# Kernel tuning notes

Measured on AMD Instinct MI355X. Metric: run time of the kernel, lower is better.

Reference implementation:

```python
import jax, jax.numpy as jnp
import numpy as np
import math

B, T, IN_DIM, HID = 32, 1024, 512, 512
TAU_MEM = 20.0
THRESHOLD = 1.0
ALPHA = math.exp(-1.0 / TAU_MEM)


def setup_inputs() -> dict:
    key = jax.random.key(0)
    kx, kw, kb = jax.random.split(key, 3)
    bound = 1.0 / math.sqrt(IN_DIM)
    x = jax.random.normal(kx, (B, T, IN_DIM), dtype=jnp.float32)
    W = jax.random.uniform(kw, (HID, IN_DIM), minval=-bound, maxval=bound, dtype=jnp.float32)
    b = jax.random.uniform(kb, (HID,), minval=-bound, maxval=bound, dtype=jnp.float32)
    threshold_adapt = jnp.ones((HID,), dtype=jnp.float32) * THRESHOLD
    return {"x": x, "W": W, "b": b, "threshold_adapt": threshold_adapt}


def reference(x, W, b, threshold_adapt):
    # Precompute the batched GEMM for all timesteps: z[b,t,h]
    z = jnp.einsum('bti,hi->bth', x, W) + b
    thr = threshold_adapt[None, :]  # [1,H]

    def step(mem, z_t):
        # leaky integrate
        mem = ALPHA * mem + z_t              # [B,H]
        spike = (mem >= thr).astype(mem.dtype)
        mem = mem * (1.0 - spike)            # hard reset
        return mem, spike

    mem0 = jnp.zeros((x.shape[0], W.shape[0]), dtype=x.dtype)
    # scan over time axis: z transposed to [T,B,H]
    mem_final, spikes = jax.lax.scan(step, mem0, jnp.swapaxes(z, 0, 1))
    spikes = jnp.swapaxes(spikes, 0, 1)      # [B,T,H]
    return spikes, mem_final
```

## Files before the change

### kernel.cpp

```cpp
#include <hip/hip_runtime.h>
#include <cstdint>
#include <cstddef>

#define BATCH  32
#define TSTEPS 1024
#define INDIM  512
#define HIDDIM 512
#define MTOT   (BATCH * TSTEPS)

#define MB 128
#define NB 128
#define KC 32
#define KTILES (INDIM / KC)
#define NBLK   (HIDDIM / NB)

constexpr float ALPHA = 0.951229424500714f;

__global__ __launch_bounds__(256)
void snn_gemm(const float* __restrict__ x, const float* __restrict__ W,
              float* __restrict__ z)
{
    __shared__ float Asm[KC][MB];
    __shared__ float Bsm[KC][NB];

    const int tid = threadIdx.x;
    const int mb  = blockIdx.x / NBLK;
    const int nb  = blockIdx.x % NBLK;
    const int m0  = mb * MB;
    const int n0  = nb * NB;

    const int sr = tid >> 1;
    const int sc = (tid & 1) * 4;

    const float4* Ag = reinterpret_cast<const float4*>(x + (size_t)(m0 + sr) * INDIM) + sc;
    const float4* Bg = reinterpret_cast<const float4*>(W + (size_t)(n0 + sr) * INDIM) + sc;

    const int cm = (tid >> 4) * 8;
    const int cn = (tid & 15) * 8;

    float acc[8][8];
#pragma unroll
    for (int i = 0; i < 8; ++i)
#pragma unroll
        for (int j = 0; j < 8; ++j) acc[i][j] = 0.0f;

    float4 sa[4], sb[4];
#pragma unroll
    for (int j = 0; j < 4; ++j) { sa[j] = Ag[j]; sb[j] = Bg[j]; }

    for (int kt = 0; kt < KTILES; ++kt) {
        __syncthreads();
#pragma unroll
        for (int j = 0; j < 4; ++j) {
            const int kq = (sc + j) * 4;
            Asm[kq + 0][sr] = sa[j].x;
            Asm[kq + 1][sr] = sa[j].y;
            Asm[kq + 2][sr] = sa[j].z;
            Asm[kq + 3][sr] = sa[j].w;
            Bsm[kq + 0][sr] = sb[j].x;
            Bsm[kq + 1][sr] = sb[j].y;
            Bsm[kq + 2][sr] = sb[j].z;
            Bsm[kq + 3][sr] = sb[j].w;
        }
        __syncthreads();

        if (kt + 1 < KTILES) {
            Ag += KC / 4;
            Bg += KC / 4;
#pragma unroll
            for (int j = 0; j < 4; ++j) { sa[j] = Ag[j]; sb[j] = Bg[j]; }
        }

#pragma unroll 8
        for (int kc = 0; kc < KC; ++kc) {
            float4 a0 = *reinterpret_cast<const float4*>(&Asm[kc][cm]);
            float4 a1 = *reinterpret_cast<const float4*>(&Asm[kc][cm + 4]);
            float4 b0 = *reinterpret_cast<const float4*>(&Bsm[kc][cn]);
            float4 b1 = *reinterpret_cast<const float4*>(&Bsm[kc][cn + 4]);
            const float av[8] = {a0.x, a0.y, a0.z, a0.w, a1.x, a1.y, a1.z, a1.w};
            const float bv[8] = {b0.x, b0.y, b0.z, b0.w, b1.x, b1.y, b1.z, b1.w};
#pragma unroll
            for (int i = 0; i < 8; ++i)
#pragma unroll
                for (int j = 0; j < 8; ++j)
                    acc[i][j] = fmaf(av[i], bv[j], acc[i][j]);
        }
    }

#pragma unroll
    for (int i = 0; i < 8; ++i) {
        float* zr = z + (size_t)(m0 + cm + i) * HIDDIM + n0 + cn;
        float4 v0 = {acc[i][0], acc[i][1], acc[i][2], acc[i][3]};
        float4 v1 = {acc[i][4], acc[i][5], acc[i][6], acc[i][7]};
        *reinterpret_cast<float4*>(zr)     = v0;
        *reinterpret_cast<float4*>(zr + 4) = v1;
    }
}

template <bool INPLACE>
__global__ __launch_bounds__(64)
void snn_scan(const float* zsrc, float* out,
              const float* __restrict__ bias, const float* __restrict__ thr)
{
    const int h = (blockIdx.x & 7) * 64 + threadIdx.x;
    const int b = blockIdx.x >> 3;

    const float bb = bias[h];
    const float tt = thr[h];
    float mem = 0.0f;

    const size_t base = ((size_t)b * TSTEPS) * HIDDIM + h;
    const float* zp = zsrc + base;
    float* sp = out + base;

    for (int t = 0; t < TSTEPS; t += 8) {
        float zl[8];
#pragma unroll
        for (int j = 0; j < 8; ++j)
            zl[j] = zp[(size_t)(t + j) * HIDDIM];
#pragma unroll
        for (int j = 0; j < 8; ++j) {
            float zv = zl[j] + bb;
            mem = fmaf(ALPHA, mem, zv);
            bool s = (mem >= tt);
            sp[(size_t)(t + j) * HIDDIM] = s ? 1.0f : 0.0f;
            mem = s ? 0.0f : mem;
        }
    }
    out[(size_t)MTOT * HIDDIM + (size_t)b * HIDDIM + h] = mem;
}

extern "C" void kernel_launch(void* const* d_in, const int* in_sizes, int n_in,
                              void* d_out, int out_size, void* d_ws, size_t ws_size,
                              hipStream_t stream)
{
    const float* x    = (const float*)d_in[0];
    const float* W    = (const float*)d_in[1];
    const float* bias = (const float*)d_in[2];
    const float* thr  = (const float*)d_in[3];
    float* out = (float*)d_out;

    (void)in_sizes; (void)n_in; (void)out_size;

    const size_t z_bytes = (size_t)MTOT * HIDDIM * sizeof(float);
    float* zbuf;
    bool use_ws = (ws_size >= z_bytes);
    zbuf = use_ws ? (float*)d_ws : out;

    dim3 ggrid((MTOT / MB) * NBLK);
    hipLaunchKernelGGL(snn_gemm, ggrid, dim3(256), 0, stream, x, W, zbuf);

    dim3 sgrid(BATCH * (HIDDIM / 64));
    if (use_ws)
        hipLaunchKernelGGL((snn_scan<false>), sgrid, dim3(64), 0, stream, zbuf, out, bias, thr);
    else
        hipLaunchKernelGGL((snn_scan<true>),  sgrid, dim3(64), 0, stream, zbuf, out, bias, thr);
}
```

Baseline: 389.9 us.

## Enlarge GEMM tile with swizzled LDS and double-buffer scan via async global-to-LDS loads

The GEMM moves to 256x128 tiles with 16x8 per-thread accumulators and XOR-swizzled shared-memory columns, cutting bank conflicts and raising arithmetic intensity per LDS read. The scan kernel becomes 256-thread blocks that prefetch 64-timestep chunks of z into LDS with global_load_lds double buffering, hiding the latency of the serial recurrence. The risks are register pressure from 128 accumulators under a 2-blocks launch bound, and far fewer scan blocks (64), which limits parallelism across the GPU.

```diff
diff --git a/kernel.cpp b/kernel.cpp
--- a/kernel.cpp
+++ b/kernel.cpp
@@ -8,79 +8,105 @@
 #define HIDDIM 512
 #define MTOT   (BATCH * TSTEPS)
 
-#define MB 128
-#define NB 128
-#define KC 32
-#define KTILES (INDIM / KC)
-#define NBLK   (HIDDIM / NB)
+#define GMB 256
+#define GNB 128
+#define GKC 32
+#define GKT (INDIM / GKC)
+#define GNBLK (HIDDIM / GNB)
+
+#define SB_H 256
+#define SB_T 64
+#define SB_NC (TSTEPS / SB_T)
 
 constexpr float ALPHA = 0.951229424500714f;
 
-__global__ __launch_bounds__(256)
+__device__ __forceinline__ int swzA(int g) { return g ^ (g >> 3); }
+__device__ __forceinline__ int swzB(int g) { return g ^ (g >> 3); }
+
+__global__ __launch_bounds__(256, 2)
 void snn_gemm(const float* __restrict__ x, const float* __restrict__ W,
               float* __restrict__ z)
 {
-    __shared__ float Asm[KC][MB];
-    __shared__ float Bsm[KC][NB];
+    __shared__ float Asm[GKC][GMB];
+    __shared__ float Bsm[GKC][GNB];
 
     const int tid = threadIdx.x;
-    const int mb  = blockIdx.x / NBLK;
-    const int nb  = blockIdx.x % NBLK;
-    const int m0  = mb * MB;
-    const int n0  = nb * NB;
-
-    const int sr = tid >> 1;
-    const int sc = (tid & 1) * 4;
-
-    const float4* Ag = reinterpret_cast<const float4*>(x + (size_t)(m0 + sr) * INDIM) + sc;
-    const float4* Bg = reinterpret_cast<const float4*>(W + (size_t)(n0 + sr) * INDIM) + sc;
-
-    const int cm = (tid >> 4) * 8;
+    const int mb  = blockIdx.x / GNBLK;
+    const int nb  = blockIdx.x % GNBLK;
+    const int m0  = mb * GMB;
+    const int n0  = nb * GNB;
+
+    const float4* Ag = reinterpret_cast<const float4*>(x + (size_t)(m0 + tid) * INDIM);
+    const int   acol = (swzA(tid >> 2) << 2) | (tid & 3);
+    const int   brow = tid & 127;
+    const int   bkq  = (tid >> 7) * 4;
+    const float4* Bg = reinterpret_cast<const float4*>(W + (size_t)(n0 + brow) * INDIM) + bkq;
+    const int   bcol = (swzB(brow >> 2) << 2) | (brow & 3);
+
+    const int cm = (tid >> 4) * 16;
     const int cn = (tid & 15) * 8;
-
-    float acc[8][8];
-#pragma unroll
-    for (int i = 0; i < 8; ++i)
+    int pa[4], pb[2];
+#pragma unroll
+    for (int i = 0; i < 4; ++i) pa[i] = swzA((cm >> 2) + i);
+#pragma unroll
+    for (int j = 0; j < 2; ++j) pb[j] = swzB((cn >> 2) + j);
+
+    float acc[16][8];
+#pragma unroll
+    for (int i = 0; i < 16; ++i)
 #pragma unroll
         for (int j = 0; j < 8; ++j) acc[i][j] = 0.0f;
 
-    float4 sa[4], sb[4];
-#pragma unroll
-    for (int j = 0; j < 4; ++j) { sa[j] = Ag[j]; sb[j] = Bg[j]; }
-
-    for (int kt = 0; kt < KTILES; ++kt) {
+    float4 sa[8], sb[4];
+#pragma unroll
+    for (int q = 0; q < 8; ++q) sa[q] = Ag[q];
+#pragma unroll
+    for (int q = 0; q < 4; ++q) sb[q] = Bg[q];
+
+    for (int kt = 0; kt < GKT; ++kt) {
         __syncthreads();
 #pragma unroll
-        for (int j = 0; j < 4; ++j) {
-            const int kq = (sc + j) * 4;
-            Asm[kq + 0][sr] = sa[j].x;
-            Asm[kq + 1][sr] = sa[j].y;
-            Asm[kq + 2][sr] = sa[j].z;
-            Asm[kq + 3][sr] = sa[j].w;
-            Bsm[kq + 0][sr] = sb[j].x;
-            Bsm[kq + 1][sr] = sb[j].y;
-            Bsm[kq + 2][sr] = sb[j].z;
-            Bsm[kq + 3][sr] = sb[j].w;
+        for (int q = 0; q < 8; ++q) {
+            const int k4 = q * 4;
+            Asm[k4 + 0][acol] = sa[q].x;
+            Asm[k4 + 1][acol] = sa[q].y;
+            Asm[k4 + 2][acol] = sa[q].z;
+            Asm[k4 + 3][acol] = sa[q].w;
+        }
+#pragma unroll
+        for (int q = 0; q < 4; ++q) {
+            const int k4 = (bkq + q) * 4;
+            Bsm[k4 + 0][bcol] = sb[q].x;
+            Bsm[k4 + 1][bcol] = sb[q].y;
+            Bsm[k4 + 2][bcol] = sb[q].z;
+            Bsm[k4 + 3][bcol] = sb[q].w;
         }
         __syncthreads();
 
-        if (kt + 1 < KTILES) {
-            Ag += KC / 4;
-            Bg += KC / 4;
-#pragma unroll
-            for (int j = 0; j < 4; ++j) { sa[j] = Ag[j]; sb[j] = Bg[j]; }
-        }
-
-#pragma unroll 8
-        for (int kc = 0; kc < KC; ++kc) {
-            float4 a0 = *reinterpret_cast<const float4*>(&Asm[kc][cm]);
-            float4 a1 = *reinterpret_cast<const float4*>(&Asm[kc][cm + 4]);
-            float4 b0 = *reinterpret_cast<const float4*>(&Bsm[kc][cn]);
-            float4 b1 = *reinterpret_cast<const float4*>(&Bsm[kc][cn + 4]);
-            const float av[8] = {a0.x, a0.y, a0.z, a0.w, a1.x, a1.y, a1.z, a1.w};
-            const float bv[8] = {b0.x, b0.y, b0.z, b0.w, b1.x, b1.y, b1.z, b1.w};
-#pragma unroll
-            for (int i = 0; i < 8; ++i)
+        if (kt + 1 < GKT) {
+            Ag += GKC / 4;
+            Bg += GKC / 4;
+#pragma unroll
+            for (int q = 0; q < 8; ++q) sa[q] = Ag[q];
+#pragma unroll
+            for (int q = 0; q < 4; ++q) sb[q] = Bg[q];
+        }
+
+#pragma unroll 4
+        for (int kc = 0; kc < GKC; ++kc) {
+            const float4* Ar = reinterpret_cast<const float4*>(&Asm[kc][0]);
+            const float4* Br = reinterpret_cast<const float4*>(&Bsm[kc][0]);
+            float4 a0 = Ar[pa[0]];
+            float4 a1 = Ar[pa[1]];
+            float4 a2 = Ar[pa[2]];
+            float4 a3 = Ar[pa[3]];
+            float4 b0 = Br[pb[0]];
+            float4 b1 = Br[pb[1]];
+            const float av[16] = {a0.x, a0.y, a0.z, a0.w, a1.x, a1.y, a1.z, a1.w,
+                                  a2.x, a2.y, a2.z, a2.w, a3.x, a3.y, a3.z, a3.w};
+            const float bv[8]  = {b0.x, b0.y, b0.z, b0.w, b1.x, b1.y, b1.z, b1.w};
+#pragma unroll
+            for (int i = 0; i < 16; ++i)
 #pragma unroll
                 for (int j = 0; j < 8; ++j)
                     acc[i][j] = fmaf(av[i], bv[j], acc[i][j]);
@@ -88,7 +114,7 @@
     }
 
 #pragma unroll
-    for (int i = 0; i < 8; ++i) {
+    for (int i = 0; i < 16; ++i) {
         float* zr = z + (size_t)(m0 + cm + i) * HIDDIM + n0 + cn;
         float4 v0 = {acc[i][0], acc[i][1], acc[i][2], acc[i][3]};
         float4 v1 = {acc[i][4], acc[i][5], acc[i][6], acc[i][7]};
@@ -97,37 +123,67 @@
     }
 }
 
-template <bool INPLACE>
-__global__ __launch_bounds__(64)
-void snn_scan(const float* zsrc, float* out,
+__global__ __launch_bounds__(256)
+void snn_scan(const float* __restrict__ zsrc, float* __restrict__ out,
               const float* __restrict__ bias, const float* __restrict__ thr)
 {
-    const int h = (blockIdx.x & 7) * 64 + threadIdx.x;
-    const int b = blockIdx.x >> 3;
-
-    const float bb = bias[h];
-    const float tt = thr[h];
+    __shared__ float zl[2][SB_T][SB_H];
+
+    const int tid  = threadIdx.x;
+    const int lane = tid & 63;
+    const int wave = tid >> 6;
+    const int b    = blockIdx.x >> 1;
+    const int h0   = (blockIdx.x & 1) * SB_H;
+
+    const float bb = bias[h0 + tid];
+    const float tt = thr[h0 + tid];
     float mem = 0.0f;
 
-    const size_t base = ((size_t)b * TSTEPS) * HIDDIM + h;
-    const float* zp = zsrc + base;
-    float* sp = out + base;
-
-    for (int t = 0; t < TSTEPS; t += 8) {
-        float zl[8];
-#pragma unroll
-        for (int j = 0; j < 8; ++j)
-            zl[j] = zp[(size_t)(t + j) * HIDDIM];
-#pragma unroll
-        for (int j = 0; j < 8; ++j) {
-            float zv = zl[j] + bb;
+    const float* zbase = zsrc + (size_t)b * TSTEPS * HIDDIM + h0;
+    float*       obase = out  + (size_t)b * TSTEPS * HIDDIM + h0;
+
+    auto issue = [&](int c, int buf) {
+        const float* gr = zbase + ((size_t)c * SB_T + wave * 16) * HIDDIM + lane * 4;
+        const float* lr = &zl[buf][wave * 16][0];
+#pragma unroll
+        for (int r = 0; r < 16; ++r) {
+            __builtin_amdgcn_global_load_lds(
+                (const __attribute__((address_space(1))) void*)gr,
+                (__attribute__((address_space(3))) void*)lr, 16, 0, 0);
+            gr += HIDDIM;
+            lr += SB_H;
+        }
+    };
+
+    issue(0, 0);
+
+    for (int c = 0; c < SB_NC; ++c) {
+        const int buf = c & 1;
+        if (c + 1 < SB_NC) {
+            issue(c + 1, buf ^ 1);
+            asm volatile("s_waitcnt vmcnt(16)" ::: "memory");
+        } else {
+            asm volatile("s_waitcnt vmcnt(0)" ::: "memory");
+        }
+        __builtin_amdgcn_sched_barrier(0);
+        __builtin_amdgcn_s_barrier();
+
+        float* orow = obase + (size_t)c * SB_T * HIDDIM + tid;
+#pragma unroll 8
+        for (int r = 0; r < SB_T; ++r) {
+            float zv = zl[buf][r][tid] + bb;
             mem = fmaf(ALPHA, mem, zv);
             bool s = (mem >= tt);
-            sp[(size_t)(t + j) * HIDDIM] = s ? 1.0f : 0.0f;
+            orow[(size_t)r * HIDDIM] = s ? 1.0f : 0.0f;
             mem = s ? 0.0f : mem;
         }
+
+        asm volatile("s_waitcnt lgkmcnt(0)" ::: "memory");
+        __builtin_amdgcn_sched_barrier(0);
+        __builtin_amdgcn_s_barrier();
     }
-    out[(size_t)MTOT * HIDDIM + (size_t)b * HIDDIM + h] = mem;
+
+    out[(size_t)MTOT * HIDDIM + (size_t)b * HIDDIM + h0 + tid] = mem;
 }
 
 extern "C" void kernel_launch(void* const* d_in, const int* in_sizes, int n_in,
@@ -143,16 +199,11 @@
     (void)in_sizes; (void)n_in; (void)out_size;
 
     const size_t z_bytes = (size_t)MTOT * HIDDIM * sizeof(float);
-    float* zbuf;
-    bool use_ws = (ws_size >= z_bytes);
-    zbuf = use_ws ? (float*)d_ws : out;
-
-    dim3 ggrid((MTOT / MB) * NBLK);
+    float* zbuf = (ws_size >= z_bytes) ? (float*)d_ws : out;
+
+    dim3 ggrid((MTOT / GMB) * GNBLK);
     hipLaunchKernelGGL(snn_gemm, ggrid, dim3(256), 0, stream, x, W, zbuf);
 
-    dim3 sgrid(BATCH * (HIDDIM / 64));
-    if (use_ws)
-        hipLaunchKernelGGL((snn_scan<false>), sgrid, dim3(64), 0, stream, zbuf, out, bias, thr);
-    else
-        hipLaunchKernelGGL((snn_scan<true>),  sgrid, dim3(64), 0, stream, zbuf, out, bias, thr);
+    dim3 sgrid(BATCH * (HIDDIM / SB_H));
+    hipLaunchKernelGGL(snn_scan, sgrid, dim3(256), 0, stream, zbuf, out, bias, thr);
 }
```

Result: faster. 374.2 us (-4.0%).

## Double-buffer GEMM LDS with swizzle and pipeline scan via async LDS loads

Applied to the files above, without the earlier changes.

The GEMM now double-buffers its shared-memory tiles, which removes one barrier per k-tile, and XOR-swizzles the LDS layout to cut bank conflicts on the transposed stores. The scan kernel now streams 64-timestep chunks of z into LDS with global_load_lds, double-buffered and governed by explicit vmcnt waits. Spikes are staged in LDS and written out as coalesced float4 rows. The scan previously ran 256 threads-per-block-equivalent strided scalar loads with little latency hiding. In exchange, the in-place fallback that wrote z into out loses its aliasing safety because restrict is now asserted, and the hand-coded waitcnt values are fragile.

```diff
diff --git a/kernel.cpp b/kernel.cpp
--- a/kernel.cpp
+++ b/kernel.cpp
@@ -11,17 +11,23 @@
 #define MB 128
 #define NB 128
 #define KC 32
-#define KTILES (INDIM / KC)
-#define NBLK   (HIDDIM / NB)
+#define KT (INDIM / KC)
+#define NBLK (HIDDIM / NB)
+
+#define SH 64
+#define ST 64
+#define SNC (TSTEPS / ST)
 
 constexpr float ALPHA = 0.951229424500714f;
+
+__device__ __forceinline__ int swzg(int g) { return g ^ (g >> 3); }
 
 __global__ __launch_bounds__(256)
 void snn_gemm(const float* __restrict__ x, const float* __restrict__ W,
               float* __restrict__ z)
 {
-    __shared__ float Asm[KC][MB];
-    __shared__ float Bsm[KC][NB];
+    __shared__ float Asm[2][KC][MB];
+    __shared__ float Bsm[2][KC][NB];
 
     const int tid = threadIdx.x;
     const int mb  = blockIdx.x / NBLK;
@@ -31,12 +37,15 @@
 
     const int sr = tid >> 1;
     const int sc = (tid & 1) * 4;
+    const int swr = (swzg(sr >> 2) << 2) | (sr & 3);
 
     const float4* Ag = reinterpret_cast<const float4*>(x + (size_t)(m0 + sr) * INDIM) + sc;
     const float4* Bg = reinterpret_cast<const float4*>(W + (size_t)(n0 + sr) * INDIM) + sc;
 
     const int cm = (tid >> 4) * 8;
     const int cn = (tid & 15) * 8;
+    const int am0 = swzg(cm >> 2), am1 = swzg((cm >> 2) + 1);
+    const int bn0 = swzg(cn >> 2), bn1 = swzg((cn >> 2) + 1);
 
     float acc[8][8];
 #pragma unroll
@@ -45,38 +54,48 @@
         for (int j = 0; j < 8; ++j) acc[i][j] = 0.0f;
 
     float4 sa[4], sb[4];
-#pragma unroll
-    for (int j = 0; j < 4; ++j) { sa[j] = Ag[j]; sb[j] = Bg[j]; }
-
-    for (int kt = 0; kt < KTILES; ++kt) {
-        __syncthreads();
-#pragma unroll
-        for (int j = 0; j < 4; ++j) {
-            const int kq = (sc + j) * 4;
-            Asm[kq + 0][sr] = sa[j].x;
-            Asm[kq + 1][sr] = sa[j].y;
-            Asm[kq + 2][sr] = sa[j].z;
-            Asm[kq + 3][sr] = sa[j].w;
-            Bsm[kq + 0][sr] = sb[j].x;
-            Bsm[kq + 1][sr] = sb[j].y;
-            Bsm[kq + 2][sr] = sb[j].z;
-            Bsm[kq + 3][sr] = sb[j].w;
-        }
-        __syncthreads();
-
-        if (kt + 1 < KTILES) {
-            Ag += KC / 4;
-            Bg += KC / 4;
-#pragma unroll
-            for (int j = 0; j < 4; ++j) { sa[j] = Ag[j]; sb[j] = Bg[j]; }
-        }
-
+
+    auto gload = [&]() {
+#pragma unroll
+        for (int q = 0; q < 4; ++q) { sa[q] = Ag[q]; sb[q] = Bg[q]; }
+        Ag += KC / 4;
+        Bg += KC / 4;
+    };
+    auto lwrite = [&](int p) {
+#pragma unroll
+        for (int q = 0; q < 4; ++q) {
+            const int kq = (sc + q) * 4;
+            Asm[p][kq + 0][swr] = sa[q].x;
+            Asm[p][kq + 1][swr] = sa[q].y;
+            Asm[p][kq + 2][swr] = sa[q].z;
+            Asm[p][kq + 3][swr] = sa[q].w;
+            Bsm[p][kq + 0][swr] = sb[q].x;
+            Bsm[p][kq + 1][swr] = sb[q].y;
+            Bsm[p][kq + 2][swr] = sb[q].z;
+            Bsm[p][kq + 3][swr] = sb[q].w;
+        }
+    };
+
+    gload();
+    lwrite(0);
+    __syncthreads();
+    gload();
+
+    for (int kt = 0; kt < KT; ++kt) {
+        const int p = kt & 1;
+        if (kt + 1 < KT) lwrite(p ^ 1);
+        if (kt + 2 < KT) gload();
+
+        const float (*Ap)[MB] = Asm[p];
+        const float (*Bp)[NB] = Bsm[p];
 #pragma unroll 8
         for (int kc = 0; kc < KC; ++kc) {
-            float4 a0 = *reinterpret_cast<const float4*>(&Asm[kc][cm]);
-            float4 a1 = *reinterpret_cast<const float4*>(&Asm[kc][cm + 4]);
-            float4 b0 = *reinterpret_cast<const float4*>(&Bsm[kc][cn]);
-            float4 b1 = *reinterpret_cast<const float4*>(&Bsm[kc][cn + 4]);
+            const float4* Ar = reinterpret_cast<const float4*>(&Ap[kc][0]);
+            const float4* Br = reinterpret_cast<const float4*>(&Bp[kc][0]);
+            float4 a0 = Ar[am0];
+            float4 a1 = Ar[am1];
+            float4 b0 = Br[bn0];
+            float4 b1 = Br[bn1];
             const float av[8] = {a0.x, a0.y, a0.z, a0.w, a1.x, a1.y, a1.z, a1.w};
             const float bv[8] = {b0.x, b0.y, b0.z, b0.w, b1.x, b1.y, b1.z, b1.w};
 #pragma unroll
@@ -85,6 +104,7 @@
                 for (int j = 0; j < 8; ++j)
                     acc[i][j] = fmaf(av[i], bv[j], acc[i][j]);
         }
+        if (kt + 1 < KT) __syncthreads();
     }
 
 #pragma unroll
@@ -97,37 +117,71 @@
     }
 }
 
-template <bool INPLACE>
 __global__ __launch_bounds__(64)
-void snn_scan(const float* zsrc, float* out,
+void snn_scan(const float* __restrict__ zsrc, float* __restrict__ out,
               const float* __restrict__ bias, const float* __restrict__ thr)
 {
-    const int h = (blockIdx.x & 7) * 64 + threadIdx.x;
-    const int b = blockIdx.x >> 3;
-
-    const float bb = bias[h];
-    const float tt = thr[h];
+    __shared__ float zl[2][ST][SH];
+    __shared__ float stile[ST][SH];
+
+    const int lane = threadIdx.x;
+    const int b    = blockIdx.x >> 3;
+    const int h0   = (blockIdx.x & 7) * SH;
+
+    const float* zbase = zsrc + (size_t)b * TSTEPS * HIDDIM + h0;
+    float*       obase = out  + (size_t)b * TSTEPS * HIDDIM + h0;
+
+    const float bb = bias[h0 + lane];
+    const float tt = thr[h0 + lane];
     float mem = 0.0f;
 
-    const size_t base = ((size_t)b * TSTEPS) * HIDDIM + h;
-    const float* zp = zsrc + base;
-    float* sp = out + base;
-
-    for (int t = 0; t < TSTEPS; t += 8) {
-        float zl[8];
-#pragma unroll
-        for (int j = 0; j < 8; ++j)
-            zl[j] = zp[(size_t)(t + j) * HIDDIM];
-#pragma unroll
-        for (int j = 0; j < 8; ++j) {
-            float zv = zl[j] + bb;
+    auto issue = [&](int c, int buf) {
+#pragma unroll
+        for (int j = 0; j < 16; ++j) {
+            const float* gr = zbase + (size_t)(c * ST + j * 4 + (lane >> 4)) * HIDDIM
+                            + (lane & 15) * 4;
+            const float* lr = &zl[buf][j * 4][0];
+            __builtin_amdgcn_global_load_lds(
+                (const __attribute__((address_space(1))) void*)gr,
+                (__attribute__((address_space(3))) void*)lr, 16, 0, 0);
+        }
+    };
+
+    issue(0, 0);
+
+    for (int c = 0; c < SNC; ++c) {
+        const int buf = c & 1;
+        if (c + 1 < SNC) issue(c + 1, buf ^ 1);
+
+        if (c == 0 || c + 1 >= SNC)
+            asm volatile("s_waitcnt vmcnt(16)" ::: "memory");
+        else
+            asm volatile("s_waitcnt vmcnt(32)" ::: "memory");
+        __builtin_amdgcn_sched_barrier(0);
+
+#pragma unroll 8
+        for (int r = 0; r < ST; ++r) {
+            float zv = zl[buf][r][lane] + bb;
             mem = fmaf(ALPHA, mem, zv);
             bool s = (mem >= tt);
-            sp[(size_t)(t + j) * HIDDIM] = s ? 1.0f : 0.0f;
+            stile[r][lane] = s ? 1.0f : 0.0f;
             mem = s ? 0.0f : mem;
         }
+
+        asm volatile("s_waitcnt lgkmcnt(0)" ::: "memory");
+        __builtin_amdgcn_sched_barrier(0);
+
+        const float* sf = &stile[0][0];
+#pragma unroll
+        for (int j = 0; j < 16; ++j) {
+            float4 v = *reinterpret_cast<const float4*>(sf + j * 256 + lane * 4);
+            float* gp = obase + (size_t)(c * ST + j * 4 + (lane >> 4)) * HIDDIM
+                      + (lane & 15) * 4;
+            *reinterpret_cast<float4*>(gp) = v;
+        }
     }
-    out[(size_t)MTOT * HIDDIM + (size_t)b * HIDDIM + h] = mem;
+
+    out[(size_t)MTOT * HIDDIM + (size_t)b * HIDDIM + h0 + lane] = mem;
 }
 
 extern "C" void kernel_launch(void* const* d_in, const int* in_sizes, int n_in,
@@ -143,16 +197,11 @@
     (void)in_sizes; (void)n_in; (void)out_size;
 
     const size_t z_bytes = (size_t)MTOT * HIDDIM * sizeof(float);
-    float* zbuf;
-    bool use_ws = (ws_size >= z_bytes);
-    zbuf = use_ws ? (float*)d_ws : out;
+    float* zbuf = (ws_size >= z_bytes) ? (float*)d_ws : out;
 
     dim3 ggrid((MTOT / MB) * NBLK);
     hipLaunchKernelGGL(snn_gemm, ggrid, dim3(256), 0, stream, x, W, zbuf);
 
-    dim3 sgrid(BATCH * (HIDDIM / 64));
-    if (use_ws)
-        hipLaunchKernelGGL((snn_scan<false>), sgrid, dim3(64), 0, stream, zbuf, out, bias, thr);
-    else
-        hipLaunchKernelGGL((snn_scan<true>),  sgrid, dim3(64), 0, stream, zbuf, out, bias, thr);
+    dim3 sgrid(BATCH * (HIDDIM / SH));
+    hipLaunchKernelGGL(snn_scan, sgrid, dim3(64), 0, stream, zbuf, out, bias, thr);
 }
```

Result: faster. 349.5 us (-10.4%).
